# Kernel tuning notes

Measured on AMD Instinct MI355X. Metric: run time of the kernel, lower is better.

## Reference

```python
import jax, jax.numpy as jnp
import numpy as np

CONF_THRESH = 0.01
IOU_THRESH = 0.5
K = 512          # fixed pre-NMS candidate count (top-K by confidence)
MAX_WH = 4096.0  # class offset for class-aware NMS (yolov5 style)
B, N, C = 16, 25200, 85  # batch, anchors (640x640 yolov5), 5+80 classes


def xywh2xyxy(b):
    xy, wh = b[..., :2], b[..., 2:4] * 0.5
    return jnp.concatenate([xy - wh, xy + wh], axis=-1)


def box_iou(a, b):
    # a: [M,4], b: [P,4] in xyxy -> [M,P]
    lt = jnp.maximum(a[:, None, :2], b[None, :, :2])
    rb = jnp.minimum(a[:, None, 2:], b[None, :, 2:])
    inter = jnp.clip(rb - lt, 0.0).prod(-1)
    area_a = (a[:, 2] - a[:, 0]) * (a[:, 3] - a[:, 1])
    area_b = (b[:, 2] - b[:, 0]) * (b[:, 3] - b[:, 1])
    return inter / (area_a[:, None] + area_b[None, :] - inter + 1e-9)


def _score_one(pred, target):
    # pred: [N, 85] = [xywh, obj, 80 class scores]
    obj = pred[:, 4]
    cls_conf = pred[:, 5:] * obj[:, None]            # obj * class prob
    conf = cls_conf.max(-1)
    cls = jnp.argmax(cls_conf, -1)
    boxes = xywh2xyxy(pred[:, :4])
    valid = (obj > CONF_THRESH) & (conf > CONF_THRESH)
    masked = jnp.where(valid, conf, -1.0)
    scores, order = jax.lax.top_k(masked, K)          # sorted desc, fixed K
    b = boxes[order]
    c = cls[order]
    v = scores > 0.0
    # class-aware NMS via coordinate offset
    off = b + c[:, None].astype(b.dtype) * MAX_WH
    iou = box_iou(off, off)                            # [K,K]
    idxs = jnp.arange(K)

    def body(i, keep):
        sup = jnp.any((iou[i] > IOU_THRESH) & keep & (idxs < i))
        return keep.at[i].set(v[i] & ~sup)

    keep = jax.lax.fori_loop(0, K, body, jnp.zeros(K, bool))

    tmask = keep & (c == target[5].astype(jnp.int32))  # correct-class kept boxes
    iou_t = box_iou(b, target[None, :4])[:, 0]         # IoU with target box
    m = jnp.where(tmask, iou_t, -1.0)
    j = jnp.argmax(m)
    return jnp.where(jnp.any(tmask), scores[j] * iou_t[j], 0.0)


def setup_inputs() -> dict:
    key = jax.random.key(0)
    k1, k2, k3, k4 = jax.random.split(key, 4)
    xy = jax.random.uniform(k1, (B, N, 2)) * 640.0
    wh = jax.random.uniform(k2, (B, N, 2)) * 160.0 + 4.0
    obj = jax.random.uniform(k3, (B, N, 1))
    cls = jax.random.uniform(k4, (B, N, C - 5))
    x = jnp.concatenate([xy, wh, obj, cls], axis=-1)
    target = jnp.array([120.0, 150.0, 360.0, 420.0, 0.9, 17.0], dtype=jnp.float32)
    return {"x": x, "target": target}


def reference(x, target):
    return jax.vmap(lambda p: _score_one(p, target))(x)  # [B]
```

## Files before the change

kernel.cpp:

```cpp
#include <hip/hip_runtime.h>
#include <stdint.h>

#pragma clang fp contract(off)

#define BB 16
#define NN 25200
#define CCH 85
#define KTOP 512
#define NBKT 1024
#define CAP 1024


__global__ __launch_bounds__(256) void k_conf(const float* __restrict__ x,
                                              float* __restrict__ conf,
                                              uint8_t* __restrict__ clsout,
                                              unsigned* __restrict__ hist) {
    __shared__ float tile[128 * CCH];
    const int blk = blockIdx.x;
    const int tid = threadIdx.x;

    const float4* src = (const float4*)x + (size_t)blk * 2720;
    float4* dst = (float4*)tile;
    for (int i = tid; i < 2720; i += 256) dst[i] = src[i];
    __syncthreads();

    const int r = tid >> 1;
    const int half = tid & 1;
    const float* row = tile + r * CCH;
    const float obj = row[4];

    float best = -1.0f;
    int bi = 0;
    const float* cp = row + 5 + half * 40;
#pragma unroll 8
    for (int j = 0; j < 40; ++j) {
        float p = cp[j] * obj;
        if (p > best) { best = p; bi = j; }
    }
    bi += half * 40;

    float ov = __shfl_xor(best, 1);
    int   oi = __shfl_xor(bi, 1);
    if (half == 0) {
        if (ov > best) { best = ov; bi = oi; }
        const int gr = blk * 128 + r;
        const bool valid = (obj > 0.01f) && (best > 0.01f);
        conf[gr] = valid ? best : -1.0f;
        clsout[gr] = (uint8_t)bi;
        if (valid) {
            const int b = gr / NN;
            int bk = (int)(best * 1024.0f);
            if (bk > NBKT - 1) bk = NBKT - 1;
            atomicAdd(&hist[b * NBKT + bk], 1u);
        }
    }
}

__global__ __launch_bounds__(1024) void k_main(const float* __restrict__ x,
                                               const float* __restrict__ target,
                                               const float* __restrict__ conf,
                                               const uint8_t* __restrict__ clsw,
                                               const unsigned* __restrict__ hist,
                                               float* __restrict__ out) {
    __shared__ union {
        unsigned long long cand[CAP];
        unsigned maskT[KTOP][16];
    } u;
    __shared__ float4 ox4[KTOP];
    __shared__ float4 bb4[KTOP];
    __shared__ float sscore[KTOP];
    __shared__ int scls[KTOP];
    __shared__ unsigned sbuf[NBKT];
    __shared__ unsigned keep_words[16];
    __shared__ unsigned long long wred[16];
    __shared__ int sh_tstar, sh_cnt;

    const int b = blockIdx.x;
    const int tid = threadIdx.x;
    const int lane = tid & 63;

    sbuf[tid] = hist[b * NBKT + tid];
    if (tid == 0) { sh_tstar = 0; sh_cnt = 0; }
    __syncthreads();
    for (int off = 1; off < NBKT; off <<= 1) {
        unsigned v = sbuf[tid];
        if (tid + off < NBKT) v += sbuf[tid + off];
        __syncthreads();
        sbuf[tid] = v;
        __syncthreads();
    }
    if (sbuf[tid] >= KTOP && (tid == NBKT - 1 || sbuf[tid + 1] < KTOP)) sh_tstar = tid;
    __syncthreads();
    const int tstar = sh_tstar;

    const float* cb = conf + (size_t)b * NN;
    for (int i = tid; i < NN; i += 1024) {
        float c = cb[i];
        bool want = false;
        if (c > 0.0f) {
            int bk = (int)(c * 1024.0f);
            if (bk > NBKT - 1) bk = NBKT - 1;
            want = (bk >= tstar);
        }
        unsigned long long bal = __ballot(want);
        int base = 0;
        if (lane == 0 && bal) base = atomicAdd(&sh_cnt, __popcll(bal));
        base = __shfl(base, 0);
        if (want) {
            int pos = base + __popcll(bal & ((1ull << lane) - 1ull));
            if (pos < CAP) {
                unsigned bits = __float_as_uint(c);
                u.cand[pos] = ((unsigned long long)bits << 32) | (unsigned)(~i);
            }
        }
    }
    __syncthreads();
    const int M = min(sh_cnt, CAP);

    unsigned long long key = (tid < M) ? u.cand[tid] : 0ull;
    __syncthreads();
    for (int kk = 2; kk <= CAP; kk <<= 1) {
        for (int j = kk >> 1; j > 0; j >>= 1) {
            unsigned long long partner;
            if (j >= 64) {
                u.cand[tid] = key;
                __syncthreads();
                partner = u.cand[tid ^ j];
                __syncthreads();
            } else {
                partner = __shfl_xor(key, j);
            }
            bool desc = (tid & kk) == 0;
            bool lower = (tid & j) == 0;
            bool take_max = (lower == desc);
            bool pg = partner > key;
            key = (take_max == pg) ? partner : key;
        }
    }

    const float tb0 = target[0], tb1 = target[1], tb2 = target[2], tb3 = target[3];
    const int tcls = (int)target[5];
    if (tid < KTOP) {
        float sc = __uint_as_float((unsigned)(key >> 32));
        unsigned idx = ~((unsigned)key);
        bool v = sc > 0.0f;
        sscore[tid] = sc;
        float X1 = 0.f, Y1 = 0.f, X2 = 0.f, Y2 = 0.f;
        int cl = 0;
        if (v) {
            const float* rw = x + ((size_t)b * NN + idx) * CCH;
            float cx = rw[0], cy = rw[1];
            float w = rw[2] * 0.5f, h = rw[3] * 0.5f;
            X1 = cx - w; Y1 = cy - h; X2 = cx + w; Y2 = cy + h;
            cl = clsw[(size_t)b * NN + idx];
        }
        bb4[tid] = make_float4(X1, Y1, X2, Y2);
        float offv = (float)cl * 4096.0f;
        ox4[tid] = make_float4(X1 + offv, Y1 + offv, X2 + offv, Y2 + offv);
        scls[tid] = cl;
    }
    __syncthreads();

    for (int p = tid; p < KTOP * 16; p += 1024) {
        int i = p & (KTOP - 1);
        int w = p >> 9;
        unsigned bits = 0u;
        if ((w << 5) < i) {
            float4 bi = ox4[i];
            float ai = (bi.z - bi.x) * (bi.w - bi.y);
            int jbase = w << 5;
            for (int jj = 0; jj < 32; ++jj) {
                int j = jbase + jj;
                float4 bj = ox4[j];
                float lx = fmaxf(bi.x, bj.x);
                float ly = fmaxf(bi.y, bj.y);
                float rx = fminf(bi.z, bj.z);
                float ry = fminf(bi.w, bj.w);
                float inter = fmaxf(rx - lx, 0.0f) * fmaxf(ry - ly, 0.0f);
                float aj = (bj.z - bj.x) * (bj.w - bj.y);
                float den = ai + aj - inter + 1e-9f;
                float iou = inter / den;
                unsigned hit = (unsigned)((j < i) & (iou > 0.5f));
                bits |= hit << jj;
            }
        }
        u.maskT[i][w] = bits;
    }
    __syncthreads();

    if (tid < 64) {
        const int l15 = lane & 15;
        unsigned keepw = 0u;
        unsigned r_cur = u.maskT[0][l15];
        float sc_cur = sscore[0];
        for (int i = 0; i < KTOP; ++i) {
            unsigned r_next = 0u; float sc_next = 0.f;
            if (i < KTOP - 1) { r_next = u.maskT[i + 1][l15]; sc_next = sscore[i + 1]; }
            unsigned long long bal = __ballot((r_cur & keepw) != 0u);
            bool sup = (bal & 0xFFFFull) != 0ull;
            bool kept = (sc_cur > 0.0f) && !sup;
            if (kept && lane == (i >> 5)) keepw |= (1u << (i & 31));
            r_cur = r_next; sc_cur = sc_next;
        }
        if (lane < 16) keep_words[lane] = keepw;
    }
    __syncthreads();

    float m = -1.0f;
    if (tid < KTOP) {
        bool kept = (keep_words[tid >> 5] >> (tid & 31)) & 1u;
        if (kept && scls[tid] == tcls) {
            float4 bx = bb4[tid];
            float lx = fmaxf(bx.x, tb0);
            float ly = fmaxf(bx.y, tb1);
            float rx = fminf(bx.z, tb2);
            float ry = fminf(bx.w, tb3);
            float inter = fmaxf(rx - lx, 0.0f) * fmaxf(ry - ly, 0.0f);
            float areab = (bx.z - bx.x) * (bx.w - bx.y);
            float areat = (tb2 - tb0) * (tb3 - tb1);
            float den = areab + areat - inter + 1e-9f;
            m = inter / den;
        }
    }
    unsigned mb = __float_as_uint(m);
    unsigned mono = (mb & 0x80000000u) ? ~mb : (mb | 0x80000000u);
    unsigned long long rk = ((unsigned long long)mono << 32) | (unsigned)(~tid);
    for (int d = 32; d > 0; d >>= 1) {
        unsigned long long o = __shfl_xor(rk, d);
        if (o > rk) rk = o;
    }
    if ((tid & 63) == 0) wred[tid >> 6] = rk;
    __syncthreads();
    if (tid == 0) {
        unsigned long long bestk = wred[0];
        for (int i = 1; i < 16; ++i)
            if (wred[i] > bestk) bestk = wred[i];
        unsigned mono2 = (unsigned)(bestk >> 32);
        unsigned mbits = (mono2 & 0x80000000u) ? (mono2 & 0x7FFFFFFFu) : ~mono2;
        float mstar = __uint_as_float(mbits);
        int j = (int)(~((unsigned)bestk));
        out[b] = (mstar >= 0.0f) ? sscore[j] * mstar : 0.0f;
    }
}

extern "C" void kernel_launch(void* const* d_in, const int* in_sizes, int n_in,
                              void* d_out, int out_size, void* d_ws, size_t ws_size,
                              hipStream_t stream) {
    const float* x = (const float*)d_in[0];
    const float* target = (const float*)d_in[1];
    float* out = (float*)d_out;

    char* ws = (char*)d_ws;
    float* conf = (float*)ws;
    unsigned* hist = (unsigned*)(ws + 1612800);
    uint8_t* clsw = (uint8_t*)(ws + 1612800 + 65536);

    hipMemsetAsync(hist, 0, BB * NBKT * sizeof(unsigned), stream);
    k_conf<<<dim3((BB * NN) / 128), dim3(256), 0, stream>>>(x, conf, clsw, hist);
    k_main<<<dim3(BB), dim3(1024), 0, stream>>>(x, target, conf, clsw, hist, out);
}
```

Measured before the change: 325.9 us.

## Split selection, IoU mask and NMS into separate kernels; per-batch shared histogram

The monolithic per-batch kernel becomes three kernels. A selection kernel builds the confidence histogram with shared-memory atomics, then picks and sorts candidates. A mask kernel computes the IoU suppression bitmask over 8×16 blocks instead of 16. A final NMS kernel runs the serial keep scan and the target match. This removes the global histogram atomics and the memset, and spreads the costly division-heavy IoU work across many more CUs. In exchange it adds kernel launches and workspace round-trips, and it reuses each batch's conf region in the workspace as scratch.

```diff
diff --git a/kernel.cpp b/kernel.cpp
--- a/kernel.cpp
+++ b/kernel.cpp
@@ -13,8 +13,7 @@
 
 __global__ __launch_bounds__(256) void k_conf(const float* __restrict__ x,
                                               float* __restrict__ conf,
-                                              uint8_t* __restrict__ clsout,
-                                              unsigned* __restrict__ hist) {
+                                              uint8_t* __restrict__ clsout) {
     __shared__ float tile[128 * CCH];
     const int blk = blockIdx.x;
     const int tid = threadIdx.x;
@@ -47,53 +46,45 @@
         const bool valid = (obj > 0.01f) && (best > 0.01f);
         conf[gr] = valid ? best : -1.0f;
         clsout[gr] = (uint8_t)bi;
-        if (valid) {
-            const int b = gr / NN;
-            int bk = (int)(best * 1024.0f);
+    }
+}
+
+__global__ __launch_bounds__(1024) void k_sel(const float* __restrict__ x,
+                                              const uint8_t* __restrict__ clsw,
+                                              char* __restrict__ ws) {
+    __shared__ unsigned hist[NBKT];
+    __shared__ unsigned long long cand[CAP];
+    __shared__ int sh_tstar, sh_cnt;
+
+    const int b = blockIdx.x;
+    const int tid = threadIdx.x;
+    const int lane = tid & 63;
+    const float* cb = (const float*)ws + (size_t)b * NN;
+
+    hist[tid] = 0u;
+    if (tid == 0) { sh_tstar = 0; sh_cnt = 0; }
+    __syncthreads();
+    for (int i = tid; i < NN; i += 1024) {
+        float c = cb[i];
+        if (c > 0.0f) {
+            int bk = (int)(c * 1024.0f);
             if (bk > NBKT - 1) bk = NBKT - 1;
-            atomicAdd(&hist[b * NBKT + bk], 1u);
-        }
-    }
-}
-
-__global__ __launch_bounds__(1024) void k_main(const float* __restrict__ x,
-                                               const float* __restrict__ target,
-                                               const float* __restrict__ conf,
-                                               const uint8_t* __restrict__ clsw,
-                                               const unsigned* __restrict__ hist,
-                                               float* __restrict__ out) {
-    __shared__ union {
-        unsigned long long cand[CAP];
-        unsigned maskT[KTOP][16];
-    } u;
-    __shared__ float4 ox4[KTOP];
-    __shared__ float4 bb4[KTOP];
-    __shared__ float sscore[KTOP];
-    __shared__ int scls[KTOP];
-    __shared__ unsigned sbuf[NBKT];
-    __shared__ unsigned keep_words[16];
-    __shared__ unsigned long long wred[16];
-    __shared__ int sh_tstar, sh_cnt;
-
-    const int b = blockIdx.x;
-    const int tid = threadIdx.x;
-    const int lane = tid & 63;
-
-    sbuf[tid] = hist[b * NBKT + tid];
-    if (tid == 0) { sh_tstar = 0; sh_cnt = 0; }
-    __syncthreads();
+            atomicAdd(&hist[bk], 1u);
+        }
+    }
+    __syncthreads();
+
     for (int off = 1; off < NBKT; off <<= 1) {
-        unsigned v = sbuf[tid];
-        if (tid + off < NBKT) v += sbuf[tid + off];
+        unsigned v = hist[tid];
+        if (tid + off < NBKT) v += hist[tid + off];
         __syncthreads();
-        sbuf[tid] = v;
+        hist[tid] = v;
         __syncthreads();
     }
-    if (sbuf[tid] >= KTOP && (tid == NBKT - 1 || sbuf[tid + 1] < KTOP)) sh_tstar = tid;
+    if (hist[tid] >= KTOP && (tid == NBKT - 1 || hist[tid + 1] < KTOP)) sh_tstar = tid;
     __syncthreads();
     const int tstar = sh_tstar;
 
-    const float* cb = conf + (size_t)b * NN;
     for (int i = tid; i < NN; i += 1024) {
         float c = cb[i];
         bool want = false;
@@ -110,22 +101,22 @@
             int pos = base + __popcll(bal & ((1ull << lane) - 1ull));
             if (pos < CAP) {
                 unsigned bits = __float_as_uint(c);
-                u.cand[pos] = ((unsigned long long)bits << 32) | (unsigned)(~i);
+                cand[pos] = ((unsigned long long)bits << 32) | (unsigned)(~i);
             }
         }
     }
     __syncthreads();
     const int M = min(sh_cnt, CAP);
 
-    unsigned long long key = (tid < M) ? u.cand[tid] : 0ull;
+    unsigned long long key = (tid < M) ? cand[tid] : 0ull;
     __syncthreads();
     for (int kk = 2; kk <= CAP; kk <<= 1) {
         for (int j = kk >> 1; j > 0; j >>= 1) {
             unsigned long long partner;
             if (j >= 64) {
-                u.cand[tid] = key;
+                cand[tid] = key;
                 __syncthreads();
-                partner = u.cand[tid ^ j];
+                partner = cand[tid ^ j];
                 __syncthreads();
             } else {
                 partner = __shfl_xor(key, j);
@@ -138,13 +129,11 @@
         }
     }
 
-    const float tb0 = target[0], tb1 = target[1], tb2 = target[2], tb3 = target[3];
-    const int tcls = (int)target[5];
+    char* base_b = ws + (size_t)b * 100800;
     if (tid < KTOP) {
         float sc = __uint_as_float((unsigned)(key >> 32));
         unsigned idx = ~((unsigned)key);
         bool v = sc > 0.0f;
-        sscore[tid] = sc;
         float X1 = 0.f, Y1 = 0.f, X2 = 0.f, Y2 = 0.f;
         int cl = 0;
         if (v) {
@@ -154,63 +143,95 @@
             X1 = cx - w; Y1 = cy - h; X2 = cx + w; Y2 = cy + h;
             cl = clsw[(size_t)b * NN + idx];
         }
-        bb4[tid] = make_float4(X1, Y1, X2, Y2);
         float offv = (float)cl * 4096.0f;
-        ox4[tid] = make_float4(X1 + offv, Y1 + offv, X2 + offv, Y2 + offv);
-        scls[tid] = cl;
-    }
-    __syncthreads();
-
-    for (int p = tid; p < KTOP * 16; p += 1024) {
-        int i = p & (KTOP - 1);
-        int w = p >> 9;
-        unsigned bits = 0u;
-        if ((w << 5) < i) {
-            float4 bi = ox4[i];
-            float ai = (bi.z - bi.x) * (bi.w - bi.y);
-            int jbase = w << 5;
-            for (int jj = 0; jj < 32; ++jj) {
-                int j = jbase + jj;
-                float4 bj = ox4[j];
-                float lx = fmaxf(bi.x, bj.x);
-                float ly = fmaxf(bi.y, bj.y);
-                float rx = fminf(bi.z, bj.z);
-                float ry = fminf(bi.w, bj.w);
-                float inter = fmaxf(rx - lx, 0.0f) * fmaxf(ry - ly, 0.0f);
-                float aj = (bj.z - bj.x) * (bj.w - bj.y);
-                float den = ai + aj - inter + 1e-9f;
-                float iou = inter / den;
-                unsigned hit = (unsigned)((j < i) & (iou > 0.5f));
-                bits |= hit << jj;
-            }
-        }
-        u.maskT[i][w] = bits;
-    }
+        ((float4*)(base_b))[tid] = make_float4(X1, Y1, X2, Y2);
+        ((float4*)(base_b + 8192))[tid] = make_float4(X1 + offv, Y1 + offv, X2 + offv, Y2 + offv);
+        ((float*)(base_b + 16384))[tid] = sc;
+        ((int*)(base_b + 18432))[tid] = cl;
+    }
+}
+
+__global__ __launch_bounds__(1024) void k_mask(char* __restrict__ ws) {
+    __shared__ float4 sox[KTOP];
+    const int slice = blockIdx.x;
+    const int b = blockIdx.y;
+    const int tid = threadIdx.x;
+    char* base_b = ws + (size_t)b * 100800;
+
+    if (tid < KTOP) sox[tid] = ((const float4*)(base_b + 8192))[tid];
+    __syncthreads();
+
+    const int i = slice * 64 + (tid >> 4);
+    const int w = tid & 15;
+    unsigned bits = 0u;
+    if ((w << 5) < i) {
+        float4 bi = sox[i];
+        float ai = (bi.z - bi.x) * (bi.w - bi.y);
+        const int jbase = w << 5;
+        for (int jj = 0; jj < 32; ++jj) {
+            int j = jbase + jj;
+            float4 bj = sox[j];
+            float lx = fmaxf(bi.x, bj.x);
+            float ly = fmaxf(bi.y, bj.y);
+            float rx = fminf(bi.z, bj.z);
+            float ry = fminf(bi.w, bj.w);
+            float inter = fmaxf(rx - lx, 0.0f) * fmaxf(ry - ly, 0.0f);
+            float aj = (bj.z - bj.x) * (bj.w - bj.y);
+            float den = ai + aj - inter + 1e-9f;
+            float iou = inter / den;
+            unsigned hit = (unsigned)((j < i) & (iou > 0.5f));
+            bits |= hit << jj;
+        }
+    }
+    ((unsigned*)(base_b + 32768))[slice * 1024 + tid] = bits;
+}
+
+__global__ __launch_bounds__(512) void k_nms(const float* __restrict__ target,
+                                             const char* __restrict__ ws,
+                                             float* __restrict__ out) {
+    __shared__ unsigned smask[KTOP][16];
+    __shared__ float4 sbb[KTOP];
+    __shared__ float sscore[KTOP];
+    __shared__ int scls[KTOP];
+    __shared__ unsigned keep_words[16];
+    __shared__ unsigned long long wred[8];
+
+    const int b = blockIdx.x;
+    const int tid = threadIdx.x;
+    const char* base_b = ws + (size_t)b * 100800;
+
+    const uint4* mg = (const uint4*)(base_b + 32768);
+    for (int p = tid; p < 2048; p += 512) ((uint4*)smask)[p] = mg[p];
+    sbb[tid] = ((const float4*)(base_b))[tid];
+    sscore[tid] = ((const float*)(base_b + 16384))[tid];
+    scls[tid] = ((const int*)(base_b + 18432))[tid];
     __syncthreads();
 
     if (tid < 64) {
-        const int l15 = lane & 15;
+        const int l15 = tid & 15;
         unsigned keepw = 0u;
-        unsigned r_cur = u.maskT[0][l15];
+        unsigned r_cur = smask[0][l15];
         float sc_cur = sscore[0];
         for (int i = 0; i < KTOP; ++i) {
             unsigned r_next = 0u; float sc_next = 0.f;
-            if (i < KTOP - 1) { r_next = u.maskT[i + 1][l15]; sc_next = sscore[i + 1]; }
+            if (i < KTOP - 1) { r_next = smask[i + 1][l15]; sc_next = sscore[i + 1]; }
             unsigned long long bal = __ballot((r_cur & keepw) != 0u);
             bool sup = (bal & 0xFFFFull) != 0ull;
             bool kept = (sc_cur > 0.0f) && !sup;
-            if (kept && lane == (i >> 5)) keepw |= (1u << (i & 31));
+            if (kept && tid == (i >> 5)) keepw |= (1u << (i & 31));
             r_cur = r_next; sc_cur = sc_next;
         }
-        if (lane < 16) keep_words[lane] = keepw;
-    }
-    __syncthreads();
-
+        if (tid < 16) keep_words[tid] = keepw;
+    }
+    __syncthreads();
+
+    const float tb0 = target[0], tb1 = target[1], tb2 = target[2], tb3 = target[3];
+    const int tcls = (int)target[5];
     float m = -1.0f;
-    if (tid < KTOP) {
+    {
         bool kept = (keep_words[tid >> 5] >> (tid & 31)) & 1u;
         if (kept && scls[tid] == tcls) {
-            float4 bx = bb4[tid];
+            float4 bx = sbb[tid];
             float lx = fmaxf(bx.x, tb0);
             float ly = fmaxf(bx.y, tb1);
             float rx = fminf(bx.z, tb2);
@@ -233,7 +254,7 @@
     __syncthreads();
     if (tid == 0) {
         unsigned long long bestk = wred[0];
-        for (int i = 1; i < 16; ++i)
+        for (int i = 1; i < 8; ++i)
             if (wred[i] > bestk) bestk = wred[i];
         unsigned mono2 = (unsigned)(bestk >> 32);
         unsigned mbits = (mono2 & 0x80000000u) ? (mono2 & 0x7FFFFFFFu) : ~mono2;
@@ -252,10 +273,10 @@
 
     char* ws = (char*)d_ws;
     float* conf = (float*)ws;
-    unsigned* hist = (unsigned*)(ws + 1612800);
-    uint8_t* clsw = (uint8_t*)(ws + 1612800 + 65536);
-
-    hipMemsetAsync(hist, 0, BB * NBKT * sizeof(unsigned), stream);
-    k_conf<<<dim3((BB * NN) / 128), dim3(256), 0, stream>>>(x, conf, clsw, hist);
-    k_main<<<dim3(BB), dim3(1024), 0, stream>>>(x, target, conf, clsw, hist, out);
-}
+    uint8_t* clsw = (uint8_t*)(ws + 1612800);
+
+    k_conf<<<dim3((BB * NN) / 128), dim3(256), 0, stream>>>(x, conf, clsw);
+    k_sel<<<dim3(BB), dim3(1024), 0, stream>>>(x, clsw, ws);
+    k_mask<<<dim3(8, BB), dim3(1024), 0, stream>>>(ws);
+    k_nms<<<dim3(BB), dim3(512), 0, stream>>>(target, ws, out);
+}
```

After: 283.3 us. 1.15x faster.

## Move histogram and argmax-class into per-batch kernel, drop memset and global atomics

Applied to the files above, without the earlier changes.

The first kernel now computes only the max confidence per anchor with branchless fmaxf, with no argmax, class write or global atomic histogram. The per-batch kernel builds the histogram in shared memory from float4 loads of conf, and recomputes the class argmax only for the 512 selected candidates. This removes the memset launch, the global atomics and the byte-wise class store across all anchors. In exchange the single-block-per-batch kernel does an extra pass over conf with shared atomics, and that pass runs on only 16 blocks.

```diff
diff --git a/kernel.cpp b/kernel.cpp
--- a/kernel.cpp
+++ b/kernel.cpp
@@ -12,9 +12,7 @@
 
 
 __global__ __launch_bounds__(256) void k_conf(const float* __restrict__ x,
-                                              float* __restrict__ conf,
-                                              uint8_t* __restrict__ clsout,
-                                              unsigned* __restrict__ hist) {
+                                              float* __restrict__ conf) {
     __shared__ float tile[128 * CCH];
     const int blk = blockIdx.x;
     const int tid = threadIdx.x;
@@ -30,47 +28,28 @@
     const float obj = row[4];
 
     float best = -1.0f;
-    int bi = 0;
     const float* cp = row + 5 + half * 40;
-#pragma unroll 8
-    for (int j = 0; j < 40; ++j) {
-        float p = cp[j] * obj;
-        if (p > best) { best = p; bi = j; }
-    }
-    bi += half * 40;
-
-    float ov = __shfl_xor(best, 1);
-    int   oi = __shfl_xor(bi, 1);
+#pragma unroll
+    for (int j = 0; j < 40; ++j) best = fmaxf(best, cp[j] * obj);
+    best = fmaxf(best, __shfl_xor(best, 1));
+
     if (half == 0) {
-        if (ov > best) { best = ov; bi = oi; }
         const int gr = blk * 128 + r;
-        const bool valid = (obj > 0.01f) && (best > 0.01f);
-        conf[gr] = valid ? best : -1.0f;
-        clsout[gr] = (uint8_t)bi;
-        if (valid) {
-            const int b = gr / NN;
-            int bk = (int)(best * 1024.0f);
-            if (bk > NBKT - 1) bk = NBKT - 1;
-            atomicAdd(&hist[b * NBKT + bk], 1u);
-        }
+        conf[gr] = ((obj > 0.01f) && (best > 0.01f)) ? best : -1.0f;
     }
 }
 
-__global__ __launch_bounds__(1024) void k_main(const float* __restrict__ x,
-                                               const float* __restrict__ target,
-                                               const float* __restrict__ conf,
-                                               const uint8_t* __restrict__ clsw,
-                                               const unsigned* __restrict__ hist,
-                                               float* __restrict__ out) {
+__global__ __launch_bounds__(1024) void k_fused(const float* __restrict__ x,
+                                                const float* __restrict__ target,
+                                                const float* __restrict__ conf,
+                                                float* __restrict__ out) {
     __shared__ union {
-        unsigned long long cand[CAP];
-        unsigned maskT[KTOP][16];
-    } u;
-    __shared__ float4 ox4[KTOP];
-    __shared__ float4 bb4[KTOP];
+        unsigned hist[NBKT];
+        unsigned mask[KTOP][16];
+    } um;
+    __shared__ unsigned long long cand[CAP];
+    __shared__ float4 sox[KTOP];
     __shared__ float sscore[KTOP];
-    __shared__ int scls[KTOP];
-    __shared__ unsigned sbuf[NBKT];
     __shared__ unsigned keep_words[16];
     __shared__ unsigned long long wred[16];
     __shared__ int sh_tstar, sh_cnt;
@@ -78,54 +57,74 @@
     const int b = blockIdx.x;
     const int tid = threadIdx.x;
     const int lane = tid & 63;
-
-    sbuf[tid] = hist[b * NBKT + tid];
+    const float4* cb4 = (const float4*)(conf + (size_t)b * NN);
+
+    um.hist[tid] = 0u;
     if (tid == 0) { sh_tstar = 0; sh_cnt = 0; }
     __syncthreads();
+    for (int i4 = tid; i4 < NN / 4; i4 += 1024) {
+        float4 c4 = cb4[i4];
+        float cs[4] = {c4.x, c4.y, c4.z, c4.w};
+#pragma unroll
+        for (int e = 0; e < 4; ++e) {
+            float c = cs[e];
+            if (c > 0.0f) {
+                int bk = (int)(c * 1024.0f);
+                if (bk > NBKT - 1) bk = NBKT - 1;
+                atomicAdd(&um.hist[bk], 1u);
+            }
+        }
+    }
+    __syncthreads();
+
     for (int off = 1; off < NBKT; off <<= 1) {
-        unsigned v = sbuf[tid];
-        if (tid + off < NBKT) v += sbuf[tid + off];
+        unsigned v = um.hist[tid];
+        if (tid + off < NBKT) v += um.hist[tid + off];
         __syncthreads();
-        sbuf[tid] = v;
+        um.hist[tid] = v;
         __syncthreads();
     }
-    if (sbuf[tid] >= KTOP && (tid == NBKT - 1 || sbuf[tid + 1] < KTOP)) sh_tstar = tid;
+    if (um.hist[tid] >= KTOP && (tid == NBKT - 1 || um.hist[tid + 1] < KTOP)) sh_tstar = tid;
     __syncthreads();
     const int tstar = sh_tstar;
 
-    const float* cb = conf + (size_t)b * NN;
-    for (int i = tid; i < NN; i += 1024) {
-        float c = cb[i];
-        bool want = false;
-        if (c > 0.0f) {
-            int bk = (int)(c * 1024.0f);
-            if (bk > NBKT - 1) bk = NBKT - 1;
-            want = (bk >= tstar);
-        }
-        unsigned long long bal = __ballot(want);
-        int base = 0;
-        if (lane == 0 && bal) base = atomicAdd(&sh_cnt, __popcll(bal));
-        base = __shfl(base, 0);
-        if (want) {
-            int pos = base + __popcll(bal & ((1ull << lane) - 1ull));
-            if (pos < CAP) {
-                unsigned bits = __float_as_uint(c);
-                u.cand[pos] = ((unsigned long long)bits << 32) | (unsigned)(~i);
+    for (int i4 = tid; i4 < NN / 4; i4 += 1024) {
+        float4 c4 = cb4[i4];
+        float cs[4] = {c4.x, c4.y, c4.z, c4.w};
+#pragma unroll
+        for (int e = 0; e < 4; ++e) {
+            float c = cs[e];
+            bool want = false;
+            if (c > 0.0f) {
+                int bk = (int)(c * 1024.0f);
+                if (bk > NBKT - 1) bk = NBKT - 1;
+                want = (bk >= tstar);
+            }
+            unsigned long long bal = __ballot(want);
+            int base = 0;
+            if (lane == 0 && bal) base = atomicAdd(&sh_cnt, __popcll(bal));
+            base = __shfl(base, 0);
+            if (want) {
+                int pos = base + __popcll(bal & ((1ull << lane) - 1ull));
+                if (pos < CAP) {
+                    unsigned bits = __float_as_uint(c);
+                    cand[pos] = ((unsigned long long)bits << 32) | (unsigned)(~(i4 * 4 + e));
+                }
             }
         }
     }
     __syncthreads();
     const int M = min(sh_cnt, CAP);
 
-    unsigned long long key = (tid < M) ? u.cand[tid] : 0ull;
+    unsigned long long key = (tid < M) ? cand[tid] : 0ull;
     __syncthreads();
     for (int kk = 2; kk <= CAP; kk <<= 1) {
         for (int j = kk >> 1; j > 0; j >>= 1) {
             unsigned long long partner;
             if (j >= 64) {
-                u.cand[tid] = key;
+                cand[tid] = key;
                 __syncthreads();
-                partner = u.cand[tid ^ j];
+                partner = cand[tid ^ j];
                 __syncthreads();
             } else {
                 partner = __shfl_xor(key, j);
@@ -137,27 +136,43 @@
             key = (take_max == pg) ? partner : key;
         }
     }
-
-    const float tb0 = target[0], tb1 = target[1], tb2 = target[2], tb3 = target[3];
-    const int tcls = (int)target[5];
-    if (tid < KTOP) {
-        float sc = __uint_as_float((unsigned)(key >> 32));
-        unsigned idx = ~((unsigned)key);
-        bool v = sc > 0.0f;
-        sscore[tid] = sc;
-        float X1 = 0.f, Y1 = 0.f, X2 = 0.f, Y2 = 0.f;
-        int cl = 0;
-        if (v) {
-            const float* rw = x + ((size_t)b * NN + idx) * CCH;
+    cand[tid] = key;
+    __syncthreads();
+
+    const int rank = tid >> 1;
+    const int half = tid & 1;
+    unsigned long long rkey = cand[rank];
+    float sc = __uint_as_float((unsigned)(rkey >> 32));
+    unsigned idx = ~((unsigned)rkey);
+    const bool v = sc > 0.0f;
+    float X1 = 0.f, Y1 = 0.f, X2 = 0.f, Y2 = 0.f;
+    int cl = 0;
+    if (v) {
+        const float* rw = x + ((size_t)b * NN + idx) * CCH;
+        const float obj = rw[4];
+        float bbest = -1.0f;
+        int bi = 0;
+        const float* cp = rw + 5 + half * 40;
+#pragma unroll 8
+        for (int j = 0; j < 40; ++j) {
+            float p = cp[j] * obj;
+            if (p > bbest) { bbest = p; bi = j; }
+        }
+        bi += half * 40;
+        float ov = __shfl_xor(bbest, 1);
+        int oi = __shfl_xor(bi, 1);
+        if (half == 0) {
+            if (ov > bbest) { bbest = ov; bi = oi; }
+            cl = bi;
             float cx = rw[0], cy = rw[1];
             float w = rw[2] * 0.5f, h = rw[3] * 0.5f;
             X1 = cx - w; Y1 = cy - h; X2 = cx + w; Y2 = cy + h;
-            cl = clsw[(size_t)b * NN + idx];
-        }
-        bb4[tid] = make_float4(X1, Y1, X2, Y2);
+        }
+    }
+    if (half == 0) {
+        sscore[rank] = sc;
         float offv = (float)cl * 4096.0f;
-        ox4[tid] = make_float4(X1 + offv, Y1 + offv, X2 + offv, Y2 + offv);
-        scls[tid] = cl;
+        sox[rank] = make_float4(X1 + offv, Y1 + offv, X2 + offv, Y2 + offv);
     }
     __syncthreads();
 
@@ -166,16 +181,16 @@
         int w = p >> 9;
         unsigned bits = 0u;
         if ((w << 5) < i) {
-            float4 bi = ox4[i];
-            float ai = (bi.z - bi.x) * (bi.w - bi.y);
-            int jbase = w << 5;
+            float4 bi4 = sox[i];
+            float ai = (bi4.z - bi4.x) * (bi4.w - bi4.y);
+            const int jbase = w << 5;
             for (int jj = 0; jj < 32; ++jj) {
                 int j = jbase + jj;
-                float4 bj = ox4[j];
-                float lx = fmaxf(bi.x, bj.x);
-                float ly = fmaxf(bi.y, bj.y);
-                float rx = fminf(bi.z, bj.z);
-                float ry = fminf(bi.w, bj.w);
+                float4 bj = sox[j];
+                float lx = fmaxf(bi4.x, bj.x);
+                float ly = fmaxf(bi4.y, bj.y);
+                float rx = fminf(bi4.z, bj.z);
+                float ry = fminf(bi4.w, bj.w);
                 float inter = fmaxf(rx - lx, 0.0f) * fmaxf(ry - ly, 0.0f);
                 float aj = (bj.z - bj.x) * (bj.w - bj.y);
                 float den = ai + aj - inter + 1e-9f;
@@ -184,39 +199,40 @@
                 bits |= hit << jj;
             }
         }
-        u.maskT[i][w] = bits;
+        um.mask[i][w] = bits;
     }
     __syncthreads();
 
     if (tid < 64) {
-        const int l15 = lane & 15;
+        const int l15 = tid & 15;
         unsigned keepw = 0u;
-        unsigned r_cur = u.maskT[0][l15];
+        unsigned r_cur = um.mask[0][l15];
         float sc_cur = sscore[0];
         for (int i = 0; i < KTOP; ++i) {
             unsigned r_next = 0u; float sc_next = 0.f;
-            if (i < KTOP - 1) { r_next = u.maskT[i + 1][l15]; sc_next = sscore[i + 1]; }
+            if (i < KTOP - 1) { r_next = um.mask[i + 1][l15]; sc_next = sscore[i + 1]; }
             unsigned long long bal = __ballot((r_cur & keepw) != 0u);
             bool sup = (bal & 0xFFFFull) != 0ull;
             bool kept = (sc_cur > 0.0f) && !sup;
-            if (kept && lane == (i >> 5)) keepw |= (1u << (i & 31));
+            if (kept && tid == (i >> 5)) keepw |= (1u << (i & 31));
             r_cur = r_next; sc_cur = sc_next;
         }
-        if (lane < 16) keep_words[lane] = keepw;
-    }
-    __syncthreads();
-
+        if (tid < 16) keep_words[tid] = keepw;
+    }
+    __syncthreads();
+
+    const float tb0 = target[0], tb1 = target[1], tb2 = target[2], tb3 = target[3];
+    const int tcls = (int)target[5];
     float m = -1.0f;
-    if (tid < KTOP) {
-        bool kept = (keep_words[tid >> 5] >> (tid & 31)) & 1u;
-        if (kept && scls[tid] == tcls) {
-            float4 bx = bb4[tid];
-            float lx = fmaxf(bx.x, tb0);
-            float ly = fmaxf(bx.y, tb1);
-            float rx = fminf(bx.z, tb2);
-            float ry = fminf(bx.w, tb3);
+    if (half == 0) {
+        bool kept = (keep_words[rank >> 5] >> (rank & 31)) & 1u;
+        if (kept && cl == tcls) {
+            float lx = fmaxf(X1, tb0);
+            float ly = fmaxf(Y1, tb1);
+            float rx = fminf(X2, tb2);
+            float ry = fminf(Y2, tb3);
             float inter = fmaxf(rx - lx, 0.0f) * fmaxf(ry - ly, 0.0f);
-            float areab = (bx.z - bx.x) * (bx.w - bx.y);
+            float areab = (X2 - X1) * (Y2 - Y1);
             float areat = (tb2 - tb0) * (tb3 - tb1);
             float den = areab + areat - inter + 1e-9f;
             m = inter / den;
@@ -224,7 +240,7 @@
     }
     unsigned mb = __float_as_uint(m);
     unsigned mono = (mb & 0x80000000u) ? ~mb : (mb | 0x80000000u);
-    unsigned long long rk = ((unsigned long long)mono << 32) | (unsigned)(~tid);
+    unsigned long long rk = ((unsigned long long)mono << 32) | (unsigned)(~rank);
     for (int d = 32; d > 0; d >>= 1) {
         unsigned long long o = __shfl_xor(rk, d);
         if (o > rk) rk = o;
@@ -249,13 +265,8 @@
     const float* x = (const float*)d_in[0];
     const float* target = (const float*)d_in[1];
     float* out = (float*)d_out;
-
-    char* ws = (char*)d_ws;
-    float* conf = (float*)ws;
-    unsigned* hist = (unsigned*)(ws + 1612800);
-    uint8_t* clsw = (uint8_t*)(ws + 1612800 + 65536);
-
-    hipMemsetAsync(hist, 0, BB * NBKT * sizeof(unsigned), stream);
-    k_conf<<<dim3((BB * NN) / 128), dim3(256), 0, stream>>>(x, conf, clsw, hist);
-    k_main<<<dim3(BB), dim3(1024), 0, stream>>>(x, target, conf, clsw, hist, out);
+    float* conf = (float*)d_ws;
+
+    k_conf<<<dim3((BB * NN) / 128), dim3(256), 0, stream>>>(x, conf);
+    k_fused<<<dim3(BB), dim3(1024), 0, stream>>>(x, target, conf, out);
 }
```

New measurement: 316.0 us. -3.0%, faster.
